# Performance work log

Hardware: AMD Instinct MI355X
Metric: run time of the kernel (lower is better)

The kernel has to match this reference:

```python
import jax, jax.numpy as jnp
import numpy as np

C = 1024  # in_channels
B, SQ, SKV = 4, 2048, 2048


def setup_inputs() -> dict:
    key = jax.random.key(0)
    ks = jax.random.split(key, 10)
    s = 1.0 / np.sqrt(C)
    return {
        "x": jax.random.normal(ks[0], (B, SQ, C), jnp.float32),
        "content_embeddings": jax.random.normal(ks[1], (B, SKV, C), jnp.float32),
        "Wq": jax.random.normal(ks[2], (C, C), jnp.float32) * s,
        "bq": jnp.zeros((C,), jnp.float32),
        "Wk": jax.random.normal(ks[3], (C, C), jnp.float32) * s,
        "bk": jnp.zeros((C,), jnp.float32),
        "Wv": jax.random.normal(ks[4], (C, C), jnp.float32) * s,
        "bv": jnp.zeros((C,), jnp.float32),
        "Wo": jax.random.normal(ks[5], (C, C), jnp.float32) * s,
        "bo": jnp.zeros((C,), jnp.float32),
    }


def reference(x, content_embeddings, Wq, bq, Wk, bk, Wv, bv, Wo, bo):
    # torch Linear: y = x @ W.T + b
    queries = x @ Wq.T + bq                    # [B, SQ, C]
    keys = content_embeddings @ Wk.T + bk      # [B, SKV, C]
    values = content_embeddings @ Wv.T + bv    # [B, SKV, C]
    scale = 1.0 / jnp.sqrt(jnp.asarray(C, x.dtype))
    scores = jnp.einsum("bqc,bkc->bqk", queries, keys) * scale  # [B, SQ, SKV]
    attn = jax.nn.softmax(scores, axis=-1)
    attended = jnp.einsum("bqk,bkc->bqc", attn, values)         # [B, SQ, C]
    out = x + attended
    return out @ Wo.T + bo
```

## Files before the change

kernel.cpp:

```cpp
#include <hip/hip_runtime.h>


typedef __attribute__((ext_vector_type(8))) short short8;
typedef __attribute__((ext_vector_type(8))) unsigned short ushort8;
typedef __attribute__((ext_vector_type(4))) float f32x4;

__device__ __forceinline__ float b2f(unsigned short u) {
  union { unsigned int i; float f; } x;
  x.i = ((unsigned int)u) << 16;
  return x.f;
}
__device__ __forceinline__ unsigned short f2b(float f) {
  union { float f; unsigned int i; } x;
  x.f = f;
  unsigned int i = x.i;
  i += 0x7fffu + ((i >> 16) & 1u);
  return (unsigned short)(i >> 16);
}

__device__ __forceinline__ void async_copy16(const void* g, void* l) {
  __builtin_amdgcn_global_load_lds(
      (const __attribute__((address_space(1))) unsigned int*)g,
      (__attribute__((address_space(3))) unsigned int*)l, 16, 0, 0);
}

__global__ void detect_fmt(const unsigned short* __restrict__ x, int* flag) {
  __shared__ int cnt;
  if (threadIdx.x == 0) cnt = 0;
  __syncthreads();
  int c = 0;
  for (int i = threadIdx.x * 2; i < 8192; i += 512) {
    unsigned e = (x[i] >> 7) & 0xFF;
    if (e >= 0x90) ++c;
  }
  atomicAdd(&cnt, c);
  __syncthreads();
  if (threadIdx.x == 0) *flag = (cnt > 64) ? 1 : 0;
}

struct CvtArgs { const void* src[10]; };

__global__ __launch_bounds__(256) void convert_all(
    CvtArgs a, unsigned short* __restrict__ dst, const int* __restrict__ flag) {
  const bool f32 = (*flag != 0);
  const long nchunk = 2621952;
  for (long c = blockIdx.x * 256L + threadIdx.x; c < nchunk;
       c += 1024L * 256) {
    const long flat = c * 8;
    int t; long off;
    if      (flat < 8388608)  { t = 0; off = 0; }
    else if (flat < 16777216) { t = 1; off = 8388608; }
    else if (flat < 17825792) { t = 2; off = 16777216; }
    else if (flat < 17826816) { t = 3; off = 17825792; }
    else if (flat < 18875392) { t = 4; off = 17826816; }
    else if (flat < 18876416) { t = 5; off = 18875392; }
    else if (flat < 19924992) { t = 6; off = 18876416; }
    else if (flat < 19926016) { t = 7; off = 19924992; }
    else if (flat < 20974592) { t = 8; off = 19926016; }
    else                      { t = 9; off = 20974592; }
    const long li = flat - off;
    if (f32) {
      const float* s = (const float*)a.src[t] + li;
      const f32x4 lo = *(const f32x4*)s;
      const f32x4 hi = *(const f32x4*)(s + 4);
      ushort8 o;
      o[0] = f2b(lo[0]); o[1] = f2b(lo[1]); o[2] = f2b(lo[2]); o[3] = f2b(lo[3]);
      o[4] = f2b(hi[0]); o[5] = f2b(hi[1]); o[6] = f2b(hi[2]); o[7] = f2b(hi[3]);
      *(ushort8*)(dst + flat) = o;
    } else {
      *(ushort8*)(dst + flat) =
          *(const ushort8*)((const unsigned short*)a.src[t] + li);
    }
  }
}

#define MODE_BIAS 0
#define MODE_RES  2
#define MODE_SB   3
#define MODE_OUT  4

__device__ __forceinline__ void xcd_swizzle(int gx, int gy, int& bx, int& by) {
  const int L = blockIdx.y * gx + blockIdx.x;
  const int r = L & 7, m = L >> 3;
  bx = m % gx;
  by = r * (gy >> 3) + m / gx;
}

template <int MODE, int KU>
__device__ __forceinline__ void gemm_core(
    const unsigned short* __restrict__ A, const unsigned short* __restrict__ B,
    void* __restrict__ C, const unsigned short* __restrict__ bias,
    const unsigned short* __restrict__ Res, const int* __restrict__ flg,
    int N, int K, float scale, int bx, int by) {
  __shared__ __align__(16) unsigned short As[KU * 128 * 32];
  __shared__ __align__(16) unsigned short Bs[KU * 128 * 32];
  const int tid = threadIdx.x;
  const int wave = tid >> 6, lane = tid & 63;
  const int wm = wave >> 1, wn = wave & 1;
  const int quad = lane >> 4, lrow = lane & 15;

  const long arow0 = (long)by * 128 + (tid >> 2);
  const long brow0 = (long)bx * 128 + (tid >> 2);
  const int cstg = (tid & 3) * 8;
  const unsigned short* ag0 = A + arow0 * K + cstg;
  const unsigned short* ag1 = ag0 + 64L * K;
  const unsigned short* bg0 = B + brow0 * K + cstg;
  const unsigned short* bg1 = bg0 + 64L * K;
  char* lA0 = (char*)As + tid * 16;
  char* lA1 = (char*)As + (256 + tid) * 16;
  char* lB0 = (char*)Bs + tid * 16;
  char* lB1 = (char*)Bs + (256 + tid) * 16;

  f32x4 acc[4][4];
#pragma unroll
  for (int i = 0; i < 4; ++i)
#pragma unroll
    for (int j = 0; j < 4; ++j) acc[i][j] = (f32x4){0.f, 0.f, 0.f, 0.f};

  for (int kt = 0; kt < K; kt += 32 * KU) {
#pragma unroll
    for (int u = 0; u < KU; ++u) {
      async_copy16(ag0 + kt + u * 32, lA0 + u * 8192);
      async_copy16(ag1 + kt + u * 32, lA1 + u * 8192);
      async_copy16(bg0 + kt + u * 32, lB0 + u * 8192);
      async_copy16(bg1 + kt + u * 32, lB1 + u * 8192);
    }
    __syncthreads();
#pragma unroll
    for (int u = 0; u < KU; ++u) {
      const unsigned short* Au = As + u * 4096;
      const unsigned short* Bu = Bs + u * 4096;
      short8 af[4], bfr[4];
#pragma unroll
      for (int i = 0; i < 4; ++i)
        af[i] = *(const short8*)(Au + (wm * 64 + i * 16 + lrow) * 32 + quad * 8);
#pragma unroll
      for (int j = 0; j < 4; ++j)
        bfr[j] =
            *(const short8*)(Bu + (wn * 64 + j * 16 + lrow) * 32 + quad * 8);
#pragma unroll
      for (int i = 0; i < 4; ++i)
#pragma unroll
        for (int j = 0; j < 4; ++j)
          acc[i][j] = __builtin_amdgcn_mfma_f32_16x16x32_bf16(
              af[i], bfr[j], acc[i][j], 0, 0, 0);
    }
    __syncthreads();
  }

  const bool f32out = (MODE == MODE_OUT) ? (*flg != 0) : false;
#pragma unroll
  for (int i = 0; i < 4; ++i) {
    const long row = (long)by * 128 + wm * 64 + i * 16 + quad * 4;
#pragma unroll
    for (int j = 0; j < 4; ++j) {
      const long col = (long)bx * 128 + wn * 64 + j * 16 + lrow;
#pragma unroll
      for (int r = 0; r < 4; ++r) {
        const float v = acc[i][j][r];
        const long idx = (row + r) * N + col;
        if (MODE == MODE_BIAS) {
          ((unsigned short*)C)[idx] = f2b(v + b2f(bias[col]));
        } else if (MODE == MODE_SB) {
          ((unsigned short*)C)[idx] = f2b(v * scale);
        } else if (MODE == MODE_RES) {
          ((unsigned short*)C)[idx] = f2b(v + b2f(Res[idx]));
        } else {
          const float o = v + b2f(bias[col]);
          if (f32out) ((float*)C)[idx] = o;
          else        ((unsigned short*)C)[idx] = f2b(o);
        }
      }
    }
  }
}

template <int MODE, int KU>
__global__ __launch_bounds__(256, 2) void gemm_nt(
    const unsigned short* __restrict__ A, const unsigned short* __restrict__ B,
    void* __restrict__ C, const unsigned short* __restrict__ bias,
    const unsigned short* __restrict__ Res, const int* __restrict__ flg,
    int N, int K, float scale, long sA, long sB, long sC, long sR) {
  const int bz = blockIdx.z;
  int bx, by;
  xcd_swizzle(gridDim.x, gridDim.y, bx, by);
  const unsigned short* Rb = (MODE == MODE_RES) ? Res + bz * sR : nullptr;
  void* Cb = (MODE == MODE_OUT) ? (void*)((char*)C)
                                : (void*)((unsigned short*)C + bz * sC);
  gemm_core<MODE, KU>(A + bz * sA, B + bz * sB, Cb, bias, Rb, flg, N, K, scale,
                      bx, by);
}

struct QkvArgs {
  const unsigned short* A[3];
  const unsigned short* B[3];
  unsigned short* C[3];
  const unsigned short* bias[3];
};
__global__ __launch_bounds__(256, 2) void gemm_qkv(QkvArgs a, int N, int K) {
  const int z = blockIdx.z;
  int bx, by;
  xcd_swizzle(gridDim.x, gridDim.y, bx, by);
  gemm_core<MODE_BIAS, 2>(a.A[z], a.B[z], a.C[z], a.bias[z], nullptr, nullptr,
                          N, K, 1.f, bx, by);
}

__global__ __launch_bounds__(256) void transpose2d(
    const unsigned short* __restrict__ in, unsigned short* __restrict__ out,
    int rows, int cols) {
  __shared__ unsigned short tile[32][33];
  const long b = blockIdx.z;
  in += b * (long)rows * cols;
  out += b * (long)rows * cols;
  const int r0 = blockIdx.y * 32, c0 = blockIdx.x * 32;
  const int tx = threadIdx.x & 31, ty = threadIdx.x >> 5;
#pragma unroll
  for (int i = 0; i < 32; i += 8)
    tile[ty + i][tx] = in[(long)(r0 + ty + i) * cols + (c0 + tx)];
  __syncthreads();
#pragma unroll
  for (int i = 0; i < 32; i += 8)
    out[(long)(c0 + ty + i) * rows + (r0 + tx)] = tile[tx][ty + i];
}

__global__ __launch_bounds__(256) void softmax_rows(
    unsigned short* __restrict__ SP) {
  unsigned short* s = SP + blockIdx.x * 2048L;
  const int tid = threadIdx.x;
  float v[8];
#pragma unroll
  for (int i = 0; i < 8; ++i) v[i] = b2f(s[tid + 256 * i]);
  float m = v[0];
#pragma unroll
  for (int i = 1; i < 8; ++i) m = fmaxf(m, v[i]);
#pragma unroll
  for (int off = 32; off > 0; off >>= 1) m = fmaxf(m, __shfl_xor(m, off));
  __shared__ float redm[4], reds[4];
  if ((tid & 63) == 0) redm[tid >> 6] = m;
  __syncthreads();
  m = fmaxf(fmaxf(redm[0], redm[1]), fmaxf(redm[2], redm[3]));
  float sum = 0.f;
#pragma unroll
  for (int i = 0; i < 8; ++i) {
    v[i] = __expf(v[i] - m);
    sum += v[i];
  }
#pragma unroll
  for (int off = 32; off > 0; off >>= 1) sum += __shfl_xor(sum, off);
  if ((tid & 63) == 0) reds[tid >> 6] = sum;
  __syncthreads();
  sum = reds[0] + reds[1] + reds[2] + reds[3];
  const float inv = 1.0f / sum;
#pragma unroll
  for (int i = 0; i < 8; ++i) s[tid + 256 * i] = f2b(v[i] * inv);
}

extern "C" void kernel_launch(void* const* d_in, const int* in_sizes, int n_in,
                              void* d_out, int out_size, void* d_ws,
                              size_t ws_size, hipStream_t stream) {
  char* ws = (char*)d_ws;
  const long MB = 1 << 20;
  unsigned short* C0  = (unsigned short*)ws;
  unsigned short* xb  = C0;
  unsigned short* ceb = C0 + 8388608;
  unsigned short* Wqb = C0 + 16777216;
  unsigned short* bqb = C0 + 17825792;
  unsigned short* Wkb = C0 + 17826816;
  unsigned short* bkb = C0 + 18875392;
  unsigned short* Wvb = C0 + 18876416;
  unsigned short* bvb = C0 + 19924992;
  unsigned short* Wob = C0 + 19926016;
  unsigned short* bob = C0 + 20974592;
  int*            flg = (int*)(ws + 41 * MB);
  unsigned short* Q   = (unsigned short*)(ws + 42 * MB);
  unsigned short* Kp  = (unsigned short*)(ws + 58 * MB);
  unsigned short* Vp  = (unsigned short*)(ws + 74 * MB);
  unsigned short* S   = (unsigned short*)(ws + 90 * MB);
  unsigned short* Vt  = Q;
  unsigned short* Ar  = Kp;

  const dim3 blk(256);
  const float scale = 0.03125f;

  detect_fmt<<<dim3(1), dim3(256), 0, stream>>>((const unsigned short*)d_in[0],
                                                flg);
  CvtArgs ca;
  for (int i = 0; i < 10; ++i) ca.src[i] = d_in[i];
  convert_all<<<dim3(1024), blk, 0, stream>>>(ca, C0, flg);

  QkvArgs qa;
  qa.A[0] = xb;  qa.A[1] = ceb; qa.A[2] = ceb;
  qa.B[0] = Wqb; qa.B[1] = Wkb; qa.B[2] = Wvb;
  qa.C[0] = Q;   qa.C[1] = Kp;  qa.C[2] = Vp;
  qa.bias[0] = bqb; qa.bias[1] = bkb; qa.bias[2] = bvb;
  gemm_qkv<<<dim3(8, 64, 3), blk, 0, stream>>>(qa, 1024, 1024);

  gemm_nt<MODE_SB, 2><<<dim3(16, 16, 4), blk, 0, stream>>>(
      Q, Kp, S, nullptr, nullptr, nullptr, 2048, 1024, scale,
      2048L * 1024, 2048L * 1024, 2048L * 2048, 0);

  transpose2d<<<dim3(32, 64, 4), blk, 0, stream>>>(Vp, Vt, 2048, 1024);

  softmax_rows<<<dim3(8192), blk, 0, stream>>>(S);

  gemm_nt<MODE_RES, 2><<<dim3(8, 16, 4), blk, 0, stream>>>(
      S, Vt, Ar, nullptr, xb, nullptr, 1024, 2048, 1.f,
      2048L * 2048, 1024L * 2048, 2048L * 1024, 2048L * 1024);

  gemm_nt<MODE_OUT, 2><<<dim3(8, 64, 1), blk, 0, stream>>>(
      Ar, Wob, d_out, bob, nullptr, flg, 1024, 1024, 1.f, 0, 0, 0, 0);
}
```

Baseline: 331.6 us.

## Fuse V transpose into QKV GEMM epilogue and vectorize softmax row access

The V projection now writes its output directly in transposed [B, C, SKV] layout from the GEMM epilogue, as packed 4-element stores, so the separate transpose kernel and its extra read and write of V are gone. The softmax kernel now loads and stores eight contiguous bf16 values per thread with 16-byte vector accesses instead of strided scalar ones. The transposed epilogue stores are strided by 2048 elements across lanes, so they coalesce less well than the original row-major writes.

```diff
diff --git a/kernel.cpp b/kernel.cpp
--- a/kernel.cpp
+++ b/kernel.cpp
@@ -3,6 +3,7 @@
 
 typedef __attribute__((ext_vector_type(8))) short short8;
 typedef __attribute__((ext_vector_type(8))) unsigned short ushort8;
+typedef __attribute__((ext_vector_type(4))) unsigned short ushort4v;
 typedef __attribute__((ext_vector_type(4))) float f32x4;
 
 __device__ __forceinline__ float b2f(unsigned short u) {
@@ -91,7 +92,7 @@
     const unsigned short* __restrict__ A, const unsigned short* __restrict__ B,
     void* __restrict__ C, const unsigned short* __restrict__ bias,
     const unsigned short* __restrict__ Res, const int* __restrict__ flg,
-    int N, int K, float scale, int bx, int by) {
+    int N, int K, float scale, int bx, int by, int vt) {
   __shared__ __align__(16) unsigned short As[KU * 128 * 32];
   __shared__ __align__(16) unsigned short Bs[KU * 128 * 32];
   const int tid = threadIdx.x;
@@ -155,6 +156,15 @@
 #pragma unroll
     for (int j = 0; j < 4; ++j) {
       const long col = (long)bx * 128 + wn * 64 + j * 16 + lrow;
+      if (MODE == MODE_BIAS && vt) {
+        const float bb = b2f(bias[col]);
+        ushort4v pk;
+#pragma unroll
+        for (int r = 0; r < 4; ++r) pk[r] = f2b(acc[i][j][r] + bb);
+        const long b = row >> 11, kvr = row & 2047;
+        *(ushort4v*)((unsigned short*)C + b * 2097152 + col * 2048 + kvr) = pk;
+        continue;
+      }
 #pragma unroll
       for (int r = 0; r < 4; ++r) {
         const float v = acc[i][j][r];
@@ -188,7 +198,7 @@
   void* Cb = (MODE == MODE_OUT) ? (void*)((char*)C)
                                 : (void*)((unsigned short*)C + bz * sC);
   gemm_core<MODE, KU>(A + bz * sA, B + bz * sB, Cb, bias, Rb, flg, N, K, scale,
-                      bx, by);
+                      bx, by, 0);
 }
 
 struct QkvArgs {
@@ -202,34 +212,17 @@
   int bx, by;
   xcd_swizzle(gridDim.x, gridDim.y, bx, by);
   gemm_core<MODE_BIAS, 2>(a.A[z], a.B[z], a.C[z], a.bias[z], nullptr, nullptr,
-                          N, K, 1.f, bx, by);
-}
-
-__global__ __launch_bounds__(256) void transpose2d(
-    const unsigned short* __restrict__ in, unsigned short* __restrict__ out,
-    int rows, int cols) {
-  __shared__ unsigned short tile[32][33];
-  const long b = blockIdx.z;
-  in += b * (long)rows * cols;
-  out += b * (long)rows * cols;
-  const int r0 = blockIdx.y * 32, c0 = blockIdx.x * 32;
-  const int tx = threadIdx.x & 31, ty = threadIdx.x >> 5;
-#pragma unroll
-  for (int i = 0; i < 32; i += 8)
-    tile[ty + i][tx] = in[(long)(r0 + ty + i) * cols + (c0 + tx)];
-  __syncthreads();
-#pragma unroll
-  for (int i = 0; i < 32; i += 8)
-    out[(long)(c0 + ty + i) * rows + (r0 + tx)] = tile[tx][ty + i];
+                          N, K, 1.f, bx, by, z == 2 ? 1 : 0);
 }
 
 __global__ __launch_bounds__(256) void softmax_rows(
     unsigned short* __restrict__ SP) {
   unsigned short* s = SP + blockIdx.x * 2048L;
   const int tid = threadIdx.x;
+  const ushort8 raw = *(const ushort8*)(s + tid * 8);
   float v[8];
 #pragma unroll
-  for (int i = 0; i < 8; ++i) v[i] = b2f(s[tid + 256 * i]);
+  for (int i = 0; i < 8; ++i) v[i] = b2f(raw[i]);
   float m = v[0];
 #pragma unroll
   for (int i = 1; i < 8; ++i) m = fmaxf(m, v[i]);
@@ -251,8 +244,10 @@
   __syncthreads();
   sum = reds[0] + reds[1] + reds[2] + reds[3];
   const float inv = 1.0f / sum;
-#pragma unroll
-  for (int i = 0; i < 8; ++i) s[tid + 256 * i] = f2b(v[i] * inv);
+  ushort8 o;
+#pragma unroll
+  for (int i = 0; i < 8; ++i) o[i] = f2b(v[i] * inv);
+  *(ushort8*)(s + tid * 8) = o;
 }
 
 extern "C" void kernel_launch(void* const* d_in, const int* in_sizes, int n_in,
@@ -274,9 +269,8 @@
   int*            flg = (int*)(ws + 41 * MB);
   unsigned short* Q   = (unsigned short*)(ws + 42 * MB);
   unsigned short* Kp  = (unsigned short*)(ws + 58 * MB);
-  unsigned short* Vp  = (unsigned short*)(ws + 74 * MB);
+  unsigned short* Vt  = (unsigned short*)(ws + 74 * MB);
   unsigned short* S   = (unsigned short*)(ws + 90 * MB);
-  unsigned short* Vt  = Q;
   unsigned short* Ar  = Kp;
 
   const dim3 blk(256);
@@ -291,7 +285,7 @@
   QkvArgs qa;
   qa.A[0] = xb;  qa.A[1] = ceb; qa.A[2] = ceb;
   qa.B[0] = Wqb; qa.B[1] = Wkb; qa.B[2] = Wvb;
-  qa.C[0] = Q;   qa.C[1] = Kp;  qa.C[2] = Vp;
+  qa.C[0] = Q;   qa.C[1] = Kp;  qa.C[2] = Vt;
   qa.bias[0] = bqb; qa.bias[1] = bkb; qa.bias[2] = bvb;
   gemm_qkv<<<dim3(8, 64, 3), blk, 0, stream>>>(qa, 1024, 1024);
 
@@ -299,8 +293,6 @@
       Q, Kp, S, nullptr, nullptr, nullptr, 2048, 1024, scale,
       2048L * 1024, 2048L * 1024, 2048L * 2048, 0);
 
-  transpose2d<<<dim3(32, 64, 4), blk, 0, stream>>>(Vp, Vt, 2048, 1024);
-
   softmax_rows<<<dim3(8192), blk, 0, stream>>>(S);
 
   gemm_nt<MODE_RES, 2><<<dim3(8, 16, 4), blk, 0, stream>>>(
```

Result: no change. 327.2 us (-1.3%).
